# Optimization experiments

Measured on AMD Instinct MI355X. Metric: run time of the kernel, lower is better.

Reference implementation:

```python
import jax, jax.numpy as jnp
import numpy as np

B, S = 4, 128          # batch, seq
IN, OUT = 1024, 1024   # perfect squares
C = 256                # compressed_feature_dim
K = 4                  # num_monarchs
NI, NO = 32, 32        # sqrt(IN), sqrt(OUT)
D1 = NI * NI * NO      # flat size of M1 per token
D2 = NO * NI * NO      # flat size of M2 per token


def setup_inputs() -> dict:
    key = jax.random.key(0)
    ks = jax.random.split(key, 20)
    s = 0.02
    return {
        "x":   jax.random.normal(ks[0], (B, S, IN), dtype=jnp.float32),
        # compressor: Linear(IN, C)
        "Wc":  jax.random.normal(ks[1], (IN, C), dtype=jnp.float32) * s,
        "bc":  jnp.zeros((C,), dtype=jnp.float32),
        # M1 generators (stacked over K experts): Linear(C,C), SiLU, Linear(C,D1)
        "W1a": jax.random.normal(ks[2], (K, C, C), dtype=jnp.float32) * s,
        "b1a": jnp.zeros((K, C), dtype=jnp.float32),
        "W1b": jax.random.normal(ks[3], (K, C, D1), dtype=jnp.float32) * s,
        "b1b": jax.random.normal(ks[4], (K, D1), dtype=jnp.float32) * s,
        # M2 generators
        "W2a": jax.random.normal(ks[5], (K, C, C), dtype=jnp.float32) * s,
        "b2a": jnp.zeros((K, C), dtype=jnp.float32),
        "W2b": jax.random.normal(ks[6], (K, C, D2), dtype=jnp.float32) * s,
        "b2b": jax.random.normal(ks[7], (K, D2), dtype=jnp.float32) * s,
        # mixer: Linear(C,C), SiLU, Linear(C,K)
        "Wm1": jax.random.normal(ks[8], (C, C), dtype=jnp.float32) * s,
        "bm1": jnp.zeros((C,), dtype=jnp.float32),
        "Wm2": jax.random.normal(ks[9], (C, K), dtype=jnp.float32) * s,
        "bm2": jnp.zeros((K,), dtype=jnp.float32),
        # biasor: Linear(C, OUT)
        "Wb":  jax.random.normal(ks[10], (C, OUT), dtype=jnp.float32) * s,
        "bb":  jnp.zeros((OUT,), dtype=jnp.float32),
        # ratio_gen: Linear(C, 1)
        "Wr":  jax.random.normal(ks[11], (C, 1), dtype=jnp.float32) * s,
        "br":  jnp.ones((1,), dtype=jnp.float32),
    }


def reference(x, Wc, bc, W1a, b1a, W1b, b1b, W2a, b2a, W2b, b2b,
              Wm1, bm1, Wm2, bm2, Wb, bb, Wr, br):
    silu = jax.nn.silu
    # compressor
    c = silu(x @ Wc + bc)                                   # [B,S,C]
    # per-expert hypernetwork generation of flat Monarch factors
    h1 = silu(jnp.einsum('bsc,kcd->kbsd', c, W1a) + b1a[:, None, None, :])
    M1s = jnp.einsum('kbsd,kde->kbse', h1, W1b) + b1b[:, None, None, :]  # [K,B,S,D1]
    h2 = silu(jnp.einsum('bsc,kcd->kbsd', c, W2a) + b2a[:, None, None, :])
    M2s = jnp.einsum('kbsd,kde->kbse', h2, W2b) + b2b[:, None, None, :]  # [K,B,S,D2]
    # softmax mixing coefficients
    coeffs = jax.nn.softmax(silu(c @ Wm1 + bm1) @ Wm2 + bm2, axis=-1)    # [B,S,K]
    M1_flat = jnp.einsum('kbsd,bsk->bsd', M1s, coeffs)      # [B,S,D1]
    M2_flat = jnp.einsum('kbsd,bsk->bsd', M2s, coeffs)      # [B,S,D2]
    # per-token Monarch matmul
    lead = x.shape[:-1]
    M1 = M1_flat.reshape(*lead, NI, NI, NO)
    M2 = M2_flat.reshape(*lead, NO, NI, NO)
    x1 = x.reshape(*lead, NI, NI)                            # [B,S,g=NI,i=NI]
    x1o = jnp.einsum('bsgi,bsgio->bsgo', x1, M1)             # [B,S,NI,NO]
    x2 = jnp.swapaxes(x1o, -1, -2)                           # [B,S,NO,NI]
    x2o = jnp.einsum('bsgi,bsgio->bsgo', x2, M2)             # [B,S,NO,NO]
    y = x2o.reshape(*lead, NO * NO)                          # [B,S,OUT]
    ratio = c @ Wr + br                                      # [B,S,1]
    return y * ratio + (c @ Wb + bb)
```

## Files before the change

### kernel.cpp

```cpp
#include <hip/hip_runtime.h>


typedef __bf16 bf16x8 __attribute__((ext_vector_type(8)));
typedef __bf16 bf16x2 __attribute__((ext_vector_type(2)));
typedef float  fx4    __attribute__((ext_vector_type(4)));

#define NN 32768

__device__ __forceinline__ unsigned short f2bf(float f) {
  union { __bf16 b; unsigned short u; } c; c.b = (__bf16)f; return c.u;
}
__device__ __forceinline__ unsigned pk2(float lo, float hi) {
  bf16x2 v; v[0] = (__bf16)lo; v[1] = (__bf16)hi;
  union { bf16x2 v; unsigned u; } c; c.v = v; return c.u;
}
__device__ __forceinline__ float b2f(unsigned short s) {
  union { unsigned u; float f; } v; v.u = ((unsigned)s) << 16; return v.f;
}
__device__ __forceinline__ void up8(uint4 h, float* f) {
  f[0] = b2f((unsigned short)(h.x & 0xFFFF)); f[1] = b2f((unsigned short)(h.x >> 16));
  f[2] = b2f((unsigned short)(h.y & 0xFFFF)); f[3] = b2f((unsigned short)(h.y >> 16));
  f[4] = b2f((unsigned short)(h.z & 0xFFFF)); f[5] = b2f((unsigned short)(h.z >> 16));
  f[6] = b2f((unsigned short)(h.w & 0xFFFF)); f[7] = b2f((unsigned short)(h.w >> 16));
}
__device__ __forceinline__ uint4 scale8(uint4 h, float cv) {
  uint4 u;
  u.x = pk2(b2f((unsigned short)(h.x & 0xFFFF)) * cv, b2f((unsigned short)(h.x >> 16)) * cv);
  u.y = pk2(b2f((unsigned short)(h.y & 0xFFFF)) * cv, b2f((unsigned short)(h.y >> 16)) * cv);
  u.z = pk2(b2f((unsigned short)(h.z & 0xFFFF)) * cv, b2f((unsigned short)(h.z >> 16)) * cv);
  u.w = pk2(b2f((unsigned short)(h.w & 0xFFFF)) * cv, b2f((unsigned short)(h.w >> 16)) * cv);
  return u;
}
__device__ __forceinline__ float silu_f(float x) { return x / (1.f + __expf(-x)); }

__device__ __forceinline__ void gl2lds16(const void* g, void* l) {
  __builtin_amdgcn_global_load_lds(
      (const __attribute__((address_space(1))) unsigned int*)g,
      (__attribute__((address_space(3))) unsigned int*)l, 16, 0, 0);
}

#define MFMA(a, b, c) __builtin_amdgcn_mfma_f32_16x16x32_bf16((a), (b), (c), 0, 0, 0)

__global__ __launch_bounds__(256) void k1_compress(
    const float* __restrict__ x, const float* __restrict__ Wc,
    const float* __restrict__ bc, uint4* __restrict__ c_u4) {
  const int tid = threadIdx.x;
  const int m0 = blockIdx.x * 64, n0 = blockIdx.y * 64;
  __shared__ uint4 As[8 * 64];
  __shared__ uint4 Bs[8 * 65];
  const bf16x8* Af = reinterpret_cast<const bf16x8*>(As);
  const bf16x8* Bf = reinterpret_cast<const bf16x8*>(Bs);
  uint2* Bs2 = reinterpret_cast<uint2*>(Bs);
  const int lane = tid & 63, w = tid >> 6;
  const int q = lane >> 4, rr = lane & 15;
  const int wm = (w >> 1) * 32, wn = (w & 1) * 32;
  const int arun = tid & 7, amb = tid >> 3;
  const int kgrp = tid & 15, colg = tid >> 4;
  fx4 a00 = 0, a01 = 0, a10 = 0, a11 = 0;
  fx4 areg[4], breg[4];

#pragma unroll
  for (int s = 0; s < 2; ++s) {
    const float* src = x + (size_t)(m0 + amb + 32 * s) * 1024 + arun * 8;
    areg[2 * s] = *(const fx4*)src;
    areg[2 * s + 1] = *(const fx4*)(src + 4);
  }
#pragma unroll
  for (int kk = 0; kk < 4; ++kk)
    breg[kk] = *(const fx4*)(Wc + (size_t)(kgrp * 4 + kk) * 256 + n0 + colg * 4);

  for (int kt = 0; kt < 16; ++kt) {
    __syncthreads();
#pragma unroll
    for (int s = 0; s < 2; ++s) {
      uint4 u;
      u.x = pk2(areg[2 * s][0], areg[2 * s][1]);
      u.y = pk2(areg[2 * s][2], areg[2 * s][3]);
      u.z = pk2(areg[2 * s + 1][0], areg[2 * s + 1][1]);
      u.w = pk2(areg[2 * s + 1][2], areg[2 * s + 1][3]);
      As[arun * 64 + amb + 32 * s] = u;
    }
#pragma unroll
    for (int j = 0; j < 4; ++j) {
      uint2 u;
      u.x = pk2(breg[0][j], breg[1][j]);
      u.y = pk2(breg[2][j], breg[3][j]);
      Bs2[(((kgrp >> 1) * 65 + colg * 4 + j) << 1) + (kgrp & 1)] = u;
    }
    __syncthreads();
    if (kt < 15) {
      const int k0 = (kt + 1) * 64;
#pragma unroll
      for (int s = 0; s < 2; ++s) {
        const float* src = x + (size_t)(m0 + amb + 32 * s) * 1024 + k0 + arun * 8;
        areg[2 * s] = *(const fx4*)src;
        areg[2 * s + 1] = *(const fx4*)(src + 4);
      }
#pragma unroll
      for (int kk = 0; kk < 4; ++kk)
        breg[kk] = *(const fx4*)(Wc + (size_t)(k0 + kgrp * 4 + kk) * 256 + n0 + colg * 4);
    }
#pragma unroll
    for (int ks = 0; ks < 2; ++ks) {
      const int roA = (ks * 4 + q) * 64, roB = (ks * 4 + q) * 65;
      bf16x8 fa0 = Af[roA + wm + rr];
      bf16x8 fa1 = Af[roA + wm + 16 + rr];
      bf16x8 fb0 = Bf[roB + wn + rr];
      bf16x8 fb1 = Bf[roB + wn + 16 + rr];
      a00 = MFMA(fa0, fb0, a00); a01 = MFMA(fa0, fb1, a01);
      a10 = MFMA(fa1, fb0, a10); a11 = MFMA(fa1, fb1, a11);
    }
  }
  __syncthreads();
  {
    const int r4 = tid >> 6, m = tid & 63;
    uint4 u; u.x = (r4 == 0) ? 0x3F80u : 0u; u.y = 0; u.z = 0; u.w = 0;
    As[r4 * 64 + m] = u;
    uint4 ub; ub.x = (r4 == 0) ? (unsigned)f2bf(bc[n0 + m]) : 0u;
    ub.y = 0; ub.z = 0; ub.w = 0;
    Bs[r4 * 65 + m] = ub;
  }
  __syncthreads();
  {
    bf16x8 fa0 = Af[q * 64 + wm + rr];
    bf16x8 fa1 = Af[q * 64 + wm + 16 + rr];
    bf16x8 fb0 = Bf[q * 65 + wn + rr];
    bf16x8 fb1 = Bf[q * 65 + wn + 16 + rr];
    a00 = MFMA(fa0, fb0, a00); a01 = MFMA(fa0, fb1, a01);
    a10 = MFMA(fa1, fb0, a10); a11 = MFMA(fa1, fb1, a11);
  }
  unsigned short* c16 = (unsigned short*)c_u4;
#pragma unroll
  for (int fi = 0; fi < 2; ++fi) {
#pragma unroll
    for (int fj = 0; fj < 2; ++fj) {
      fx4 v = (fi == 0) ? (fj == 0 ? a00 : a01) : (fj == 0 ? a10 : a11);
      const int cc = n0 + wn + fj * 16 + rr;
#pragma unroll
      for (int reg = 0; reg < 4; ++reg) {
        const int t = m0 + wm + fi * 16 + q * 4 + reg;
        c16[((size_t)(cc >> 3) * 512 + t) * 8 + (cc & 7)] = f2bf(silu_f(v[reg]));
      }
    }
  }
  if (blockIdx.y == 0) {
    const int r4 = tid >> 6, m = tid & 63;
    uint4 u; u.x = (r4 == 0) ? 0x3F80u : 0u; u.y = 0; u.z = 0; u.w = 0;
    c_u4[(size_t)(32 + r4) * 512 + m0 + m] = u;
  }
}

__global__ __launch_bounds__(256) void k2_hyper(
    const uint4* __restrict__ c_u4,
    const float* __restrict__ W1a, const float* __restrict__ b1a,
    const float* __restrict__ W2a, const float* __restrict__ b2a,
    const float* __restrict__ Wm1, const float* __restrict__ bm1,
    const float* __restrict__ Wb, const float* __restrict__ bb,
    unsigned short* __restrict__ H, float* __restrict__ biasout) {
  const int tid = threadIdx.x;
  const int m0 = blockIdx.x * 64, n0 = blockIdx.y * 64;
  __shared__ uint4 As[2][8 * 64];
  __shared__ uint4 Bs[8 * 65];
  const bf16x8* Bf = reinterpret_cast<const bf16x8*>(Bs);
  uint2* Bs2 = reinterpret_cast<uint2*>(Bs);
  const int lane = tid & 63, w = tid >> 6;
  const int q = lane >> 4, rr = lane & 15;
  const int wm = (w >> 1) * 32, wn = (w & 1) * 32;
  const int kgrp = tid & 15, colg = tid >> 4;

  const float* bbase; const float* biasv; int bstride;
  if (n0 < 1024) {
    const int kx = n0 >> 8;
    bbase = W1a + (size_t)kx * 65536 + (n0 & 255); bstride = 256;
    biasv = b1a + kx * 256 + (n0 & 255);
  } else if (n0 < 2048) {
    const int mm = n0 - 1024; const int kx = mm >> 8;
    bbase = W2a + (size_t)kx * 65536 + (mm & 255); bstride = 256;
    biasv = b2a + kx * 256 + (mm & 255);
  } else if (n0 < 2304) {
    bbase = Wm1 + (n0 - 2048); bstride = 256; biasv = bm1 + (n0 - 2048);
  } else {
    bbase = Wb + (n0 - 2304); bstride = 1024; biasv = bb + (n0 - 2304);
  }

  fx4 a00 = 0, a01 = 0, a10 = 0, a11 = 0;
  fx4 breg[4];
#pragma unroll
  for (int kk = 0; kk < 4; ++kk)
    breg[kk] = *(const fx4*)(bbase + (size_t)(kgrp * 4 + kk) * bstride + colg * 4);
#pragma unroll
  for (int s = 0; s < 2; ++s) {
    const int run = w * 2 + s;
    gl2lds16(c_u4 + (size_t)run * 512 + m0 + lane, (void*)(&As[0][run * 64]));
  }
  int cur = 0;
  for (int kt = 0; kt < 4; ++kt) {
    __syncthreads();
#pragma unroll
    for (int j = 0; j < 4; ++j) {
      uint2 u;
      u.x = pk2(breg[0][j], breg[1][j]);
      u.y = pk2(breg[2][j], breg[3][j]);
      Bs2[(((kgrp >> 1) * 65 + colg * 4 + j) << 1) + (kgrp & 1)] = u;
    }
    __syncthreads();
    if (kt < 3) {
#pragma unroll
      for (int s = 0; s < 2; ++s) {
        const int run = w * 2 + s;
        gl2lds16(c_u4 + (size_t)((kt + 1) * 8 + run) * 512 + m0 + lane,
                 (void*)(&As[cur ^ 1][run * 64]));
      }
#pragma unroll
      for (int kk = 0; kk < 4; ++kk)
        breg[kk] = *(const fx4*)(bbase + (size_t)((kt + 1) * 64 + kgrp * 4 + kk) * bstride + colg * 4);
    }
    const bf16x8* Af = reinterpret_cast<const bf16x8*>(As[cur]);
#pragma unroll
    for (int ks = 0; ks < 2; ++ks) {
      const int roA = (ks * 4 + q) * 64, roB = (ks * 4 + q) * 65;
      bf16x8 fa0 = Af[roA + wm + rr];
      bf16x8 fa1 = Af[roA + wm + 16 + rr];
      bf16x8 fb0 = Bf[roB + wn + rr];
      bf16x8 fb1 = Bf[roB + wn + 16 + rr];
      a00 = MFMA(fa0, fb0, a00); a01 = MFMA(fa0, fb1, a01);
      a10 = MFMA(fa1, fb0, a10); a11 = MFMA(fa1, fb1, a11);
    }
    cur ^= 1;
  }
  __syncthreads();
  {
    gl2lds16(c_u4 + (size_t)(32 + w) * 512 + m0 + lane, (void*)(&As[0][w * 64]));
    const int r4 = tid >> 6, col = tid & 63;
    uint4 ub; ub.x = (r4 == 0) ? (unsigned)f2bf(biasv[col]) : 0u;
    ub.y = 0; ub.z = 0; ub.w = 0;
    Bs[r4 * 65 + col] = ub;
  }
  __syncthreads();
  {
    const bf16x8* Af = reinterpret_cast<const bf16x8*>(As[0]);
    bf16x8 fa0 = Af[q * 64 + wm + rr];
    bf16x8 fa1 = Af[q * 64 + wm + 16 + rr];
    bf16x8 fb0 = Bf[q * 65 + wn + rr];
    bf16x8 fb1 = Bf[q * 65 + wn + 16 + rr];
    a00 = MFMA(fa0, fb0, a00); a01 = MFMA(fa0, fb1, a01);
    a10 = MFMA(fa1, fb0, a10); a11 = MFMA(fa1, fb1, a11);
  }
#pragma unroll
  for (int fi = 0; fi < 2; ++fi) {
#pragma unroll
    for (int fj = 0; fj < 2; ++fj) {
      fx4 v = (fi == 0) ? (fj == 0 ? a00 : a01) : (fj == 0 ? a10 : a11);
      const int cc = n0 + wn + fj * 16 + rr;
#pragma unroll
      for (int reg = 0; reg < 4; ++reg) {
        const int t = m0 + wm + fi * 16 + q * 4 + reg;
        if (n0 < 2304)
          H[(((size_t)(cc >> 3) * 512 + t) << 3) + (cc & 7)] = f2bf(silu_f(v[reg]));
        else
          biasout[(size_t)t * 1024 + (cc - 2304)] = v[reg];
      }
    }
  }
}

__global__ __launch_bounds__(256) void k3_prep(
    const uint4* __restrict__ Hu, const uint4* __restrict__ c_u4,
    const float* __restrict__ Wm2, const float* __restrict__ bm2,
    const float* __restrict__ Wr, const float* __restrict__ br,
    uint4* __restrict__ G1u, uint4* __restrict__ G2u, float* __restrict__ ratio) {
  const int tid = threadIdx.x;
  const int tg = blockIdx.x & 7, dgrp = blockIdx.x >> 3;
  const int t0 = tg * 64;
  __shared__ float sWm2[1024];
  __shared__ float sWr[256];
  __shared__ float part[64][4][4];
  __shared__ float rp[64][4];
  __shared__ float cf[64][4];
  ((fx4*)sWm2)[tid] = ((const fx4*)Wm2)[tid];
  if (tid < 64) ((fx4*)sWr)[tid] = ((const fx4*)Wr)[tid];
  __syncthreads();
  const int tl = tid >> 2, kx = tid & 3;
  {
    float pe0 = 0, pe1 = 0, pe2 = 0, pe3 = 0, pr = 0;
#pragma unroll
    for (int i = 0; i < 8; ++i) {
      uint4 h  = Hu[(size_t)(256 + kx * 8 + i) * 512 + t0 + tl];
      uint4 cu = c_u4[(size_t)(kx * 8 + i) * 512 + t0 + tl];
      float hf[8], cv[8];
      up8(h, hf); up8(cu, cv);
#pragma unroll
      for (int j = 0; j < 8; ++j) {
        const int ch = kx * 64 + i * 8 + j;
        pe0 += hf[j] * sWm2[ch * 4 + 0];
        pe1 += hf[j] * sWm2[ch * 4 + 1];
        pe2 += hf[j] * sWm2[ch * 4 + 2];
        pe3 += hf[j] * sWm2[ch * 4 + 3];
        pr  += cv[j] * sWr[ch];
      }
    }
    part[tl][kx][0] = pe0; part[tl][kx][1] = pe1;
    part[tl][kx][2] = pe2; part[tl][kx][3] = pe3;
    rp[tl][kx] = pr;
  }
  __syncthreads();
  if (tid < 64) {
    float l[4];
#pragma unroll
    for (int e = 0; e < 4; ++e)
      l[e] = part[tid][0][e] + part[tid][1][e] + part[tid][2][e] + part[tid][3][e] + bm2[e];
    float m = fmaxf(fmaxf(l[0], l[1]), fmaxf(l[2], l[3]));
    float e0 = __expf(l[0] - m), e1 = __expf(l[1] - m);
    float e2 = __expf(l[2] - m), e3 = __expf(l[3] - m);
    float den = e0 + e1 + e2 + e3;
    cf[tid][0] = e0 / den; cf[tid][1] = e1 / den;
    cf[tid][2] = e2 / den; cf[tid][3] = e3 / den;
    if (dgrp == 0)
      ratio[t0 + tid] = rp[tid][0] + rp[tid][1] + rp[tid][2] + rp[tid][3] + br[0];
  }
  __syncthreads();
  const int tl2 = tid & 63, sub = tid >> 6;
#pragma unroll
  for (int i = 0; i < 4; ++i) {
    const int dg = dgrp * 16 + sub * 4 + i;
    const float cv = cf[tl2][dg >> 5];
    uint4 h1 = Hu[(size_t)dg * 512 + t0 + tl2];
    G1u[(size_t)dg * 512 + t0 + tl2] = scale8(h1, cv);
    uint4 h2 = Hu[(size_t)(128 + dg) * 512 + t0 + tl2];
    G2u[(size_t)dg * 512 + t0 + tl2] = scale8(h2, cv);
  }
  if (dgrp == 0) {
    if (tid < 64) {
      uint4 u;
      u.x = pk2(cf[tid][0], cf[tid][1]);
      u.y = pk2(cf[tid][2], cf[tid][3]);
      u.z = 0; u.w = 0;
      G1u[(size_t)128 * 512 + t0 + tid] = u;
      G2u[(size_t)128 * 512 + t0 + tid] = u;
    } else {
      const int idx = tid - 64;
      uint4 z; z.x = 0; z.y = 0; z.z = 0; z.w = 0;
      G1u[(size_t)(129 + (idx >> 6)) * 512 + t0 + (idx & 63)] = z;
      G2u[(size_t)(129 + (idx >> 6)) * 512 + t0 + (idx & 63)] = z;
    }
  }
}

__global__ __launch_bounds__(256) void k_biggemm(
    const uint4* __restrict__ Gu, const float* __restrict__ W,
    const float* __restrict__ bvec, unsigned short* __restrict__ Mout) {
  const int tid = threadIdx.x;
  const int p = blockIdx.x;
  const int xcd = p & 7, slot = p >> 3;
  const int m0 = (slot & 3) * 128;
  const int n0 = ((slot >> 2) * 8 + xcd) * 128;
  __shared__ uint4 Bs[2][8 * 129];
  const int lane = tid & 63, w = tid >> 6;
  const int q = lane >> 4, rr = lane & 15;
  const int wm = (w >> 1) * 64, wn = (w & 1) * 64;
  const int bcg = tid >> 3;
  const int br  = tid & 7;
  const float* wptr = W + n0 + bcg * 4;
  const uint4* aptr = Gu + m0 + wm + rr;

  fx4 acc[4][4];
#pragma unroll
  for (int i = 0; i < 4; ++i)
#pragma unroll
    for (int j = 0; j < 4; ++j) acc[i][j] = 0;

  fx4 breg[8];
  uint4 a_cur[4], a_nxt[4];
#pragma unroll
  for (int kk = 0; kk < 8; ++kk)
    breg[kk] = *(const fx4*)(wptr + (size_t)(br * 8 + kk) * NN);
#pragma unroll
  for (int j = 0; j < 4; ++j) {
    uint4 u;
    u.x = pk2(breg[0][j], breg[1][j]); u.y = pk2(breg[2][j], breg[3][j]);
    u.z = pk2(breg[4][j], breg[5][j]); u.w = pk2(breg[6][j], breg[7][j]);
    Bs[0][br * 129 + bcg * 4 + j] = u;
  }
#pragma unroll
  for (int kk = 0; kk < 8; ++kk)
    breg[kk] = *(const fx4*)(wptr + (size_t)(64 + br * 8 + kk) * NN);
#pragma unroll
  for (int f = 0; f < 4; ++f) a_cur[f] = aptr[(size_t)q * 512 + f * 16];
  __syncthreads();

  for (int kt = 0; kt < 16; ++kt) {
    const int cur = kt & 1;
    const bf16x8* Bf = reinterpret_cast<const bf16x8*>(Bs[cur]);
    if (kt < 15) {
#pragma unroll
      for (int j = 0; j < 4; ++j) {
        uint4 u;
        u.x = pk2(breg[0][j], breg[1][j]); u.y = pk2(breg[2][j], breg[3][j]);
        u.z = pk2(breg[4][j], breg[5][j]); u.w = pk2(breg[6][j], breg[7][j]);
        Bs[cur ^ 1][br * 129 + bcg * 4 + j] = u;
      }
      if (kt < 14) {
#pragma unroll
        for (int kk = 0; kk < 8; ++kk)
          breg[kk] = *(const fx4*)(wptr + (size_t)((kt + 2) * 64 + br * 8 + kk) * NN);
      }
    }
#pragma unroll
    for (int ks = 0; ks < 2; ++ks) {
      if (kt < 15 || ks < 1) {
        const int nk8 = (ks == 0) ? (kt * 8 + 4 + q) : ((kt + 1) * 8 + q);
#pragma unroll
        for (int f = 0; f < 4; ++f) a_nxt[f] = aptr[(size_t)nk8 * 512 + f * 16];
      }
      bf16x8 b[4];
      const int roB = (ks * 4 + q) * 129;
#pragma unroll
      for (int f = 0; f < 4; ++f) b[f] = Bf[roB + wn + f * 16 + rr];
#pragma unroll
      for (int fi = 0; fi < 4; ++fi) {
        bf16x8 af = *reinterpret_cast<bf16x8*>(&a_cur[fi]);
#pragma unroll
        for (int fj = 0; fj < 4; ++fj) acc[fi][fj] = MFMA(af, b[fj], acc[fi][fj]);
      }
#pragma unroll
      for (int f = 0; f < 4; ++f) a_cur[f] = a_nxt[f];
    }
    __syncthreads();
  }
  {
#pragma unroll
    for (int f = 0; f < 4; ++f) a_cur[f] = aptr[(size_t)(128 + q) * 512 + f * 16];
    const int colB = tid & 127, half = tid >> 7;
    if (half == 0) {
#pragma unroll
      for (int r = 0; r < 4; ++r) {
        float v8[8];
#pragma unroll
        for (int j = 0; j < 8; ++j) {
          const int kk = r * 8 + j;
          v8[j] = (kk < 4) ? bvec[(size_t)kk * NN + n0 + colB] : 0.f;
        }
        uint4 u; u.x = pk2(v8[0], v8[1]); u.y = pk2(v8[2], v8[3]);
        u.z = pk2(v8[4], v8[5]); u.w = pk2(v8[6], v8[7]);
        Bs[0][r * 129 + colB] = u;
      }
    }
    __syncthreads();
    const bf16x8* Bf0 = reinterpret_cast<const bf16x8*>(Bs[0]);
    bf16x8 b[4];
#pragma unroll
    for (int f = 0; f < 4; ++f) b[f] = Bf0[q * 129 + wn + f * 16 + rr];
#pragma unroll
    for (int fi = 0; fi < 4; ++fi) {
      bf16x8 af = *reinterpret_cast<bf16x8*>(&a_cur[fi]);
#pragma unroll
      for (int fj = 0; fj < 4; ++fj) acc[fi][fj] = MFMA(af, b[fj], acc[fi][fj]);
    }
  }
#pragma unroll
  for (int fi = 0; fi < 4; ++fi) {
    const int tb = m0 + wm + fi * 16 + q * 4;
#pragma unroll
    for (int fj = 0; fj < 4; ++fj) {
      const fx4 v = acc[fi][fj];
      const int cc = n0 + wn + fj * 16 + rr;
      const int pc = ((cc >> 5) & 31) * 1024 + (cc >> 10) * 32 + (cc & 31);
#pragma unroll
      for (int reg = 0; reg < 4; ++reg)
        Mout[(size_t)(tb + reg) * NN + pc] = f2bf(v[reg]);
    }
  }
}

__global__ __launch_bounds__(256) void k_monarch1(
    const float* __restrict__ x, const unsigned short* __restrict__ M1p,
    float* __restrict__ XT) {
  const int tt = blockIdx.x, tid = threadIdx.x;
  const int h = tid >> 7, t2 = tid & 127;
  __shared__ float xs[1024];
  __shared__ float xo[2][1024];
  *(float4*)&xs[tid * 4] = *(const float4*)&x[(size_t)tt * 1024 + tid * 4];
  __syncthreads();
  const int g = t2 >> 2, ob = (t2 & 3) * 8;
  const unsigned short* mrow =
      M1p + (size_t)tt * NN + (size_t)h * 16 * 1024 + g * 32 + ob;
  float acc[8] = {0, 0, 0, 0, 0, 0, 0, 0};
#pragma unroll
  for (int i = 0; i < 16; ++i) {
    uint4 mv = *(const uint4*)&mrow[(size_t)i * 1024];
    float mf[8]; up8(mv, mf);
    const float xv = xs[g * 32 + h * 16 + i];
#pragma unroll
    for (int j = 0; j < 8; ++j) acc[j] += xv * mf[j];
  }
#pragma unroll
  for (int j = 0; j < 8; ++j) xo[h][(ob + j) * 32 + g] = acc[j];
  __syncthreads();
  {
    const int base = tid * 4;
    float4 v0 = *(const float4*)&xo[0][base];
    float4 v1 = *(const float4*)&xo[1][base];
    float4 o; o.x = v0.x + v1.x; o.y = v0.y + v1.y;
    o.z = v0.z + v1.z; o.w = v0.w + v1.w;
    *(float4*)&XT[(size_t)tt * 1024 + base] = o;
  }
}

__global__ __launch_bounds__(256) void k_monarch2(
    const unsigned short* __restrict__ M2p, const float* __restrict__ XT,
    const float* __restrict__ biasout, const float* __restrict__ ratio,
    float* __restrict__ out) {
  const int tt = blockIdx.x, tid = threadIdx.x;
  const int h = tid >> 7, t2 = tid & 127;
  __shared__ float xs[1024];
  __shared__ float xo[2][1024];
  *(float4*)&xs[tid * 4] = *(const float4*)&XT[(size_t)tt * 1024 + tid * 4];
  __syncthreads();
  const int g = t2 >> 2, ob = (t2 & 3) * 8;
  const unsigned short* mrow =
      M2p + (size_t)tt * NN + (size_t)h * 16 * 1024 + g * 32 + ob;
  float acc[8] = {0, 0, 0, 0, 0, 0, 0, 0};
#pragma unroll
  for (int i = 0; i < 16; ++i) {
    uint4 mv = *(const uint4*)&mrow[(size_t)i * 1024];
    float mf[8]; up8(mv, mf);
    const float xv = xs[g * 32 + h * 16 + i];
#pragma unroll
    for (int j = 0; j < 8; ++j) acc[j] += xv * mf[j];
  }
#pragma unroll
  for (int j = 0; j < 8; ++j) xo[h][g * 32 + ob + j] = acc[j];
  __syncthreads();
  {
    const float r = ratio[tt];
    const int base = tid * 4;
    float4 v0 = *(const float4*)&xo[0][base];
    float4 v1 = *(const float4*)&xo[1][base];
    float4 bo = *(const float4*)&biasout[(size_t)tt * 1024 + base];
    float4 o;
    o.x = (v0.x + v1.x) * r + bo.x; o.y = (v0.y + v1.y) * r + bo.y;
    o.z = (v0.z + v1.z) * r + bo.z; o.w = (v0.w + v1.w) * r + bo.w;
    *(float4*)&out[(size_t)tt * 1024 + base] = o;
  }
}

extern "C" void kernel_launch(void* const* d_in, const int* in_sizes, int n_in,
                              void* d_out, int out_size, void* d_ws, size_t ws_size,
                              hipStream_t stream) {
  (void)in_sizes; (void)n_in; (void)out_size; (void)ws_size;
  const float* x   = (const float*)d_in[0];
  const float* Wc  = (const float*)d_in[1];
  const float* bc  = (const float*)d_in[2];
  const float* W1a = (const float*)d_in[3];
  const float* b1a = (const float*)d_in[4];
  const float* W1b = (const float*)d_in[5];
  const float* b1b = (const float*)d_in[6];
  const float* W2a = (const float*)d_in[7];
  const float* b2a = (const float*)d_in[8];
  const float* W2b = (const float*)d_in[9];
  const float* b2b = (const float*)d_in[10];
  const float* Wm1 = (const float*)d_in[11];
  const float* bm1 = (const float*)d_in[12];
  const float* Wm2 = (const float*)d_in[13];
  const float* bm2 = (const float*)d_in[14];
  const float* Wb  = (const float*)d_in[15];
  const float* bb  = (const float*)d_in[16];
  const float* Wr  = (const float*)d_in[17];
  const float* br  = (const float*)d_in[18];
  float* out = (float*)d_out;

  char* ws = (char*)d_ws;
  uint4* c_u4            = (uint4*)(ws + 0);
  unsigned short* H      = (unsigned short*)(ws + 294912);
  float* biasout         = (float*)(ws + 2654208);
  uint4* G1u             = (uint4*)(ws + 4751360);
  uint4* G2u             = (uint4*)(ws + 5832704);
  float* ratio           = (float*)(ws + 6914048);
  float* XT              = (float*)(ws + 6918144);
  unsigned short* M      = (unsigned short*)(ws + 9015296);

  k1_compress<<<dim3(8, 4), 256, 0, stream>>>(x, Wc, bc, c_u4);
  k2_hyper<<<dim3(8, 52), 256, 0, stream>>>(c_u4, W1a, b1a, W2a, b2a, Wm1, bm1,
                                            Wb, bb, H, biasout);
  k3_prep<<<64, 256, 0, stream>>>((const uint4*)H, c_u4, Wm2, bm2, Wr, br,
                                  G1u, G2u, ratio);
  k_biggemm<<<1024, 256, 0, stream>>>(G1u, W1b, b1b, M);
  k_monarch1<<<512, 256, 0, stream>>>(x, M, XT);
  k_biggemm<<<1024, 256, 0, stream>>>(G2u, W2b, b2b, M);
  k_monarch2<<<512, 256, 0, stream>>>(M, XT, biasout, ratio, out);
}
```

Baseline: 471.2 us.

## Pre-convert fp32 weights to packed bf16 and stage GEMM tiles via direct LDS loads

Adds a prepass kernel that converts the large fp32 W1b/W2b weight and bias tensors into a packed bf16 k-octet layout in workspace. The big GEMM then loads both A and B tiles straight into shared memory with global-to-LDS copies, which removes the in-loop fp32 loads, packing and register double buffering. The cost is an extra full read of the fp32 weights plus a bf16 write and re-read per GEMM, and the main loop is now single-buffered with two barriers per step.

```diff
diff --git a/kernel.cpp b/kernel.cpp
--- a/kernel.cpp
+++ b/kernel.cpp
@@ -346,22 +346,59 @@
   }
 }
 
+__global__ __launch_bounds__(256) void k_prepass(
+    const float* __restrict__ W, const float* __restrict__ bvec,
+    uint4* __restrict__ Wu) {
+  const int b = blockIdx.x, tid = threadIdx.x;
+  if (b < 4096) {
+    const int oct = b >> 5;
+    const int n = (b & 31) * 1024 + tid * 4;
+    fx4 v[8];
+#pragma unroll
+    for (int k = 0; k < 8; ++k)
+      v[k] = *(const fx4*)(W + (size_t)(oct * 8 + k) * NN + n);
+#pragma unroll
+    for (int j = 0; j < 4; ++j) {
+      uint4 u;
+      u.x = pk2(v[0][j], v[1][j]); u.y = pk2(v[2][j], v[3][j]);
+      u.z = pk2(v[4][j], v[5][j]); u.w = pk2(v[6][j], v[7][j]);
+      Wu[(size_t)oct * NN + n + j] = u;
+    }
+  } else {
+    const int n = (b - 4096) * 1024 + tid * 4;
+    fx4 b0 = *(const fx4*)(bvec + n);
+    fx4 b1 = *(const fx4*)(bvec + NN + n);
+    fx4 b2 = *(const fx4*)(bvec + 2 * (size_t)NN + n);
+    fx4 b3 = *(const fx4*)(bvec + 3 * (size_t)NN + n);
+    uint4 z; z.x = 0; z.y = 0; z.z = 0; z.w = 0;
+#pragma unroll
+    for (int j = 0; j < 4; ++j) {
+      uint4 u;
+      u.x = pk2(b0[j], b1[j]); u.y = pk2(b2[j], b3[j]);
+      u.z = 0; u.w = 0;
+      Wu[(size_t)128 * NN + n + j] = u;
+      Wu[(size_t)129 * NN + n + j] = z;
+      Wu[(size_t)130 * NN + n + j] = z;
+      Wu[(size_t)131 * NN + n + j] = z;
+    }
+  }
+}
+
 __global__ __launch_bounds__(256) void k_biggemm(
-    const uint4* __restrict__ Gu, const float* __restrict__ W,
-    const float* __restrict__ bvec, unsigned short* __restrict__ Mout) {
+    const uint4* __restrict__ Gu, const uint4* __restrict__ Wu,
+    unsigned short* __restrict__ Mout) {
   const int tid = threadIdx.x;
   const int p = blockIdx.x;
   const int xcd = p & 7, slot = p >> 3;
   const int m0 = (slot & 3) * 128;
   const int n0 = ((slot >> 2) * 8 + xcd) * 128;
-  __shared__ uint4 Bs[2][8 * 129];
+  __shared__ uint4 As[8 * 128];
+  __shared__ uint4 Bs[8 * 128];
+  const bf16x8* Af = reinterpret_cast<const bf16x8*>(As);
+  const bf16x8* Bf = reinterpret_cast<const bf16x8*>(Bs);
   const int lane = tid & 63, w = tid >> 6;
   const int q = lane >> 4, rr = lane & 15;
   const int wm = (w >> 1) * 64, wn = (w & 1) * 64;
-  const int bcg = tid >> 3;
-  const int br  = tid & 7;
-  const float* wptr = W + n0 + bcg * 4;
-  const uint4* aptr = Gu + m0 + wm + rr;
 
   fx4 acc[4][4];
 #pragma unroll
@@ -369,93 +406,57 @@
 #pragma unroll
     for (int j = 0; j < 4; ++j) acc[i][j] = 0;
 
-  fx4 breg[8];
-  uint4 a_cur[4], a_nxt[4];
-#pragma unroll
-  for (int kk = 0; kk < 8; ++kk)
-    breg[kk] = *(const fx4*)(wptr + (size_t)(br * 8 + kk) * NN);
-#pragma unroll
-  for (int j = 0; j < 4; ++j) {
-    uint4 u;
-    u.x = pk2(breg[0][j], breg[1][j]); u.y = pk2(breg[2][j], breg[3][j]);
-    u.z = pk2(breg[4][j], breg[5][j]); u.w = pk2(breg[6][j], breg[7][j]);
-    Bs[0][br * 129 + bcg * 4 + j] = u;
-  }
-#pragma unroll
-  for (int kk = 0; kk < 8; ++kk)
-    breg[kk] = *(const fx4*)(wptr + (size_t)(64 + br * 8 + kk) * NN);
-#pragma unroll
-  for (int f = 0; f < 4; ++f) a_cur[f] = aptr[(size_t)q * 512 + f * 16];
-  __syncthreads();
-
   for (int kt = 0; kt < 16; ++kt) {
-    const int cur = kt & 1;
-    const bf16x8* Bf = reinterpret_cast<const bf16x8*>(Bs[cur]);
-    if (kt < 15) {
-#pragma unroll
-      for (int j = 0; j < 4; ++j) {
-        uint4 u;
-        u.x = pk2(breg[0][j], breg[1][j]); u.y = pk2(breg[2][j], breg[3][j]);
-        u.z = pk2(breg[4][j], breg[5][j]); u.w = pk2(breg[6][j], breg[7][j]);
-        Bs[cur ^ 1][br * 129 + bcg * 4 + j] = u;
-      }
-      if (kt < 14) {
-#pragma unroll
-        for (int kk = 0; kk < 8; ++kk)
-          breg[kk] = *(const fx4*)(wptr + (size_t)((kt + 2) * 64 + br * 8 + kk) * NN);
-      }
-    }
+    __syncthreads();
+#pragma unroll
+    for (int s = 0; s < 8; ++s) {
+      const int ch = w * 8 + s;
+      const int run = (ch >> 1) & 7, h = ch & 1;
+      if (ch < 16)
+        gl2lds16(Gu + (size_t)(kt * 8 + run) * 512 + m0 + h * 64 + lane,
+                 (void*)(As + run * 128 + h * 64));
+      else
+        gl2lds16(Wu + (size_t)(kt * 8 + run) * NN + n0 + h * 64 + lane,
+                 (void*)(Bs + run * 128 + h * 64));
+    }
+    __syncthreads();
 #pragma unroll
     for (int ks = 0; ks < 2; ++ks) {
-      if (kt < 15 || ks < 1) {
-        const int nk8 = (ks == 0) ? (kt * 8 + 4 + q) : ((kt + 1) * 8 + q);
-#pragma unroll
-        for (int f = 0; f < 4; ++f) a_nxt[f] = aptr[(size_t)nk8 * 512 + f * 16];
-      }
-      bf16x8 b[4];
-      const int roB = (ks * 4 + q) * 129;
-#pragma unroll
-      for (int f = 0; f < 4; ++f) b[f] = Bf[roB + wn + f * 16 + rr];
-#pragma unroll
-      for (int fi = 0; fi < 4; ++fi) {
-        bf16x8 af = *reinterpret_cast<bf16x8*>(&a_cur[fi]);
-#pragma unroll
-        for (int fj = 0; fj < 4; ++fj) acc[fi][fj] = MFMA(af, b[fj], acc[fi][fj]);
-      }
-#pragma unroll
-      for (int f = 0; f < 4; ++f) a_cur[f] = a_nxt[f];
-    }
-    __syncthreads();
-  }
-  {
-#pragma unroll
-    for (int f = 0; f < 4; ++f) a_cur[f] = aptr[(size_t)(128 + q) * 512 + f * 16];
-    const int colB = tid & 127, half = tid >> 7;
-    if (half == 0) {
-#pragma unroll
-      for (int r = 0; r < 4; ++r) {
-        float v8[8];
-#pragma unroll
-        for (int j = 0; j < 8; ++j) {
-          const int kk = r * 8 + j;
-          v8[j] = (kk < 4) ? bvec[(size_t)kk * NN + n0 + colB] : 0.f;
-        }
-        uint4 u; u.x = pk2(v8[0], v8[1]); u.y = pk2(v8[2], v8[3]);
-        u.z = pk2(v8[4], v8[5]); u.w = pk2(v8[6], v8[7]);
-        Bs[0][r * 129 + colB] = u;
-      }
-    }
-    __syncthreads();
-    const bf16x8* Bf0 = reinterpret_cast<const bf16x8*>(Bs[0]);
-    bf16x8 b[4];
-#pragma unroll
-    for (int f = 0; f < 4; ++f) b[f] = Bf0[q * 129 + wn + f * 16 + rr];
-#pragma unroll
-    for (int fi = 0; fi < 4; ++fi) {
-      bf16x8 af = *reinterpret_cast<bf16x8*>(&a_cur[fi]);
-#pragma unroll
-      for (int fj = 0; fj < 4; ++fj) acc[fi][fj] = MFMA(af, b[fj], acc[fi][fj]);
-    }
+      bf16x8 a[4], bfr[4];
+      const int ro = (ks * 4 + q) * 128;
+#pragma unroll
+      for (int f = 0; f < 4; ++f) a[f] = Af[ro + wm + f * 16 + rr];
+#pragma unroll
+      for (int f = 0; f < 4; ++f) bfr[f] = Bf[ro + wn + f * 16 + rr];
+#pragma unroll
+      for (int fi = 0; fi < 4; ++fi)
+#pragma unroll
+        for (int fj = 0; fj < 4; ++fj) acc[fi][fj] = MFMA(a[fi], bfr[fj], acc[fi][fj]);
+    }
+  }
+  __syncthreads();
+#pragma unroll
+  for (int s = 0; s < 4; ++s) {
+    const int ch = w * 4 + s;
+    const int run = (ch >> 1) & 3, h = ch & 1;
+    if (ch < 8)
+      gl2lds16(Gu + (size_t)(128 + run) * 512 + m0 + h * 64 + lane,
+               (void*)(As + run * 128 + h * 64));
+    else
+      gl2lds16(Wu + (size_t)(128 + run) * NN + n0 + h * 64 + lane,
+               (void*)(Bs + run * 128 + h * 64));
+  }
+  __syncthreads();
+  {
+    bf16x8 a[4], bfr[4];
+#pragma unroll
+    for (int f = 0; f < 4; ++f) a[f] = Af[q * 128 + wm + f * 16 + rr];
+#pragma unroll
+    for (int f = 0; f < 4; ++f) bfr[f] = Bf[q * 128 + wn + f * 16 + rr];
+#pragma unroll
+    for (int fi = 0; fi < 4; ++fi)
+#pragma unroll
+      for (int fj = 0; fj < 4; ++fj) acc[fi][fj] = MFMA(a[fi], bfr[fj], acc[fi][fj]);
   }
 #pragma unroll
   for (int fi = 0; fi < 4; ++fi) {
@@ -578,14 +579,17 @@
   float* ratio           = (float*)(ws + 6914048);
   float* XT              = (float*)(ws + 6918144);
   unsigned short* M      = (unsigned short*)(ws + 9015296);
+  uint4* Wu              = (uint4*)(ws + 42569728);
 
   k1_compress<<<dim3(8, 4), 256, 0, stream>>>(x, Wc, bc, c_u4);
   k2_hyper<<<dim3(8, 52), 256, 0, stream>>>(c_u4, W1a, b1a, W2a, b2a, Wm1, bm1,
                                             Wb, bb, H, biasout);
   k3_prep<<<64, 256, 0, stream>>>((const uint4*)H, c_u4, Wm2, bm2, Wr, br,
                                   G1u, G2u, ratio);
-  k_biggemm<<<1024, 256, 0, stream>>>(G1u, W1b, b1b, M);
+  k_prepass<<<4128, 256, 0, stream>>>(W1b, b1b, Wu);
+  k_biggemm<<<1024, 256, 0, stream>>>(G1u, Wu, M);
   k_monarch1<<<512, 256, 0, stream>>>(x, M, XT);
-  k_biggemm<<<1024, 256, 0, stream>>>(G2u, W2b, b2b, M);
+  k_prepass<<<4128, 256, 0, stream>>>(W2b, b2b, Wu);
+  k_biggemm<<<1024, 256, 0, stream>>>(G2u, Wu, M);
   k_monarch2<<<512, 256, 0, stream>>>(M, XT, biasout, ratio, out);
 }
```

Result: no change. 474.7 us (+0.7%).
